# Kernel tuning notes

Hardware: AMD Instinct MI355X
Metric: run time of the kernel (lower is better)

## Reference

```python
import math
import jax, jax.numpy as jnp
import numpy as np

MODEL_DIM = 2048
NUM_HEADS = 16
HEAD_DIM = MODEL_DIM // NUM_HEADS
B, T = 4, 2048


def setup_inputs() -> dict:
    key = jax.random.key(0)
    ks = jax.random.split(key, 9)
    s = 0.02
    d = MODEL_DIM
    return {
        "x": jax.random.normal(ks[0], (B, T, d), dtype=jnp.float32),
        "wq": jax.random.normal(ks[1], (d, d), dtype=jnp.float32) * s,
        "bq": jnp.zeros((d,), dtype=jnp.float32),
        "wk": jax.random.normal(ks[2], (d, d), dtype=jnp.float32) * s,
        "bk": jnp.zeros((d,), dtype=jnp.float32),
        "wv": jax.random.normal(ks[3], (d, d), dtype=jnp.float32) * s,
        "bv": jnp.zeros((d,), dtype=jnp.float32),
        "wo": jax.random.normal(ks[4], (d, d), dtype=jnp.float32) * s,
        "bo": jnp.zeros((d,), dtype=jnp.float32),
    }


def reference(x, wq, bq, wk, bk, wv, bv, wo, bo):
    b, t, d = x.shape
    h, hd = NUM_HEADS, HEAD_DIM
    scale = 1.0 / math.sqrt(hd)
    # torch Linear: y = x @ W^T + b
    q = (x @ wq.T + bq).reshape(b, t, h, hd).transpose(0, 2, 1, 3)  # [B,H,T,hd]
    k = (x @ wk.T + bk).reshape(b, t, h, hd).transpose(0, 2, 1, 3)
    v = (x @ wv.T + bv).reshape(b, t, h, hd).transpose(0, 2, 1, 3)
    scores = jnp.einsum("bhqd,bhkd->bhqk", q, k) * scale  # [B,H,T,T]
    mask = jnp.tril(jnp.ones((t, t), dtype=bool))
    scores = jnp.where(mask[None, None], scores, -jnp.inf)
    probs = jax.nn.softmax(scores, axis=-1)
    out = jnp.einsum("bhqk,bhkd->bhqd", probs, v)  # [B,H,T,hd]
    out = out.transpose(0, 2, 1, 3).reshape(b, t, d)
    out = out @ wo.T + bo
    return (out, k, v)
```

## Files before the change

kernel.cpp:

```cpp
#include <hip/hip_runtime.h>
#include <hip/hip_bf16.h>
#include <stdint.h>

typedef __attribute__((ext_vector_type(8))) short short8;
typedef __attribute__((ext_vector_type(4))) float f32x4;

#define DEVI __device__ __forceinline__

DEVI unsigned short f2bf(float f) {
  union { float f; unsigned int u; } c; c.f = f;
  unsigned int u = c.u;
  u += 0x7fffu + ((u >> 16) & 1u);
  return (unsigned short)(u >> 16);
}

DEVI void gl_lds16(const void* gsrc, void* lds) {
  __builtin_amdgcn_global_load_lds(
      (const __attribute__((address_space(1))) unsigned int*)gsrc,
      (__attribute__((address_space(3))) unsigned int*)lds, 16, 0, 0);
}

#define MFMA(a, b, c) __builtin_amdgcn_mfma_f32_16x16x32_bf16((a), (b), (c), 0, 0, 0)
#define BAR()  __builtin_amdgcn_s_barrier()
#define SCHED0() __builtin_amdgcn_sched_barrier(0)

__global__ void cvt_f32_bf16(const float* __restrict__ in,
                             unsigned short* __restrict__ out, int n4) {
  const int stride = gridDim.x * blockDim.x;
  for (int i = blockIdx.x * blockDim.x + threadIdx.x; i < n4; i += stride) {
    const float4 v = ((const float4*)in)[i];
    ushort4 o;
    o.x = f2bf(v.x); o.y = f2bf(v.y); o.z = f2bf(v.z); o.w = f2bf(v.w);
    ((ushort4*)out)[i] = o;
  }
}

__global__ void cvt_w4(const float* __restrict__ w0, const float* __restrict__ w1,
                       const float* __restrict__ w2, const float* __restrict__ w3,
                       unsigned short* __restrict__ o0, unsigned short* __restrict__ o1,
                       unsigned short* __restrict__ o2, unsigned short* __restrict__ o3,
                       int n4) {
  const int sel = blockIdx.y;
  const float* in = sel == 0 ? w0 : sel == 1 ? w1 : sel == 2 ? w2 : w3;
  unsigned short* out = sel == 0 ? o0 : sel == 1 ? o1 : sel == 2 ? o2 : o3;
  const int stride = gridDim.x * blockDim.x;
  for (int i = blockIdx.x * blockDim.x + threadIdx.x; i < n4; i += stride) {
    const float4 v = ((const float4*)in)[i];
    ushort4 o;
    o.x = f2bf(v.x); o.y = f2bf(v.y); o.z = f2bf(v.z); o.w = f2bf(v.w);
    ((ushort4*)out)[i] = o;
  }
}


template<int MODE>
__global__ __launch_bounds__(512, 2)
void gemm8p(const unsigned short* __restrict__ A,
            const unsigned short* __restrict__ Bw,
            const float* __restrict__ bq,
            const float* __restrict__ bk,
            const float* __restrict__ bv,
            float* __restrict__ Kf,
            float* __restrict__ Vf,
            unsigned short* __restrict__ Qpk,
            unsigned short* __restrict__ Kpk,
            unsigned short* __restrict__ Vpk,
            float* __restrict__ Cf,
            int M, int N, int K)
{
  __shared__ unsigned short S[2][32768];
  const int tid  = threadIdx.x;
  const int lane = tid & 63;
  const int wid  = tid >> 6;
  const int l15  = lane & 15, l4 = lane >> 4;
  const int wm   = wid >> 2, wn = wid & 3;

  const int chunk = gridDim.x >> 3;
  const int q  = blockIdx.x;
  const int wg = (q & 7) * chunk + (q >> 3);
  const int bm = (wg & 31) * 256;
  const int bn = (wg >> 5) * 256;

  const unsigned short* Asrc = A  + (size_t)(bm + (wid >> 1) * 16 + l15) * K + (wid & 1) * 32 + l4 * 8;
  const unsigned short* Bsrc = Bw + (size_t)(bn + (wid >> 1) * 16 + l15) * K + (wid & 1) * 32 + l4 * 8;

  const int nKt   = K >> 6;
  const int HTmax = nKt * 4;

  auto stage_ht = [&](int g) {
    if (g >= HTmax) return;
    const int t = g >> 2, sub = g & 3, buf = t & 1, k0 = t << 6;
#pragma unroll
    for (int cc = 0; cc < 2; ++cc) {
      if (sub >= 2) {
        const int c = (sub - 2) * 2 + cc;
        gl_lds16(Asrc + (size_t)(c * 64) * K + k0,
                 &S[buf][c * 4096 + wid * 512 + lane * 8]);
      } else {
        const int c = sub * 2 + cc;
        gl_lds16(Bsrc + (size_t)(c * 64) * K + k0,
                 &S[buf][16384 + c * 4096 + wid * 512 + lane * 8]);
      }
    }
  };

#pragma unroll
  for (int g = 0; g < 7; ++g) stage_ht(g);
  asm volatile("s_waitcnt vmcnt(6)" ::: "memory");
  SCHED0();
  BAR();

  f32x4 acc[8][4] = {};
  short8 a[4][2], b[4][2];

  for (int t = 0; t < nKt; ++t) {
    const unsigned short* Sb = S[t & 1];
    const int P = t * 4;

#pragma unroll
    for (int i = 0; i < 4; ++i)
#pragma unroll
      for (int ks = 0; ks < 2; ++ks)
        a[i][ks] = *(const short8*)&Sb[((wm * 8 + i) * 2 + ks) * 512 + lane * 8];
#pragma unroll
    for (int j = 0; j < 4; ++j)
#pragma unroll
      for (int ks = 0; ks < 2; ++ks)
        b[j][ks] = *(const short8*)&Sb[16384 + ((wn * 4 + j) * 2 + ks) * 512 + lane * 8];
    stage_ht(P + 7);
    BAR();
    asm volatile("s_waitcnt lgkmcnt(0)" ::: "memory");
    SCHED0();
    __builtin_amdgcn_s_setprio(1);
#pragma unroll
    for (int i = 0; i < 4; ++i)
#pragma unroll
      for (int j = 0; j < 2; ++j)
#pragma unroll
        for (int ks = 0; ks < 2; ++ks)
          acc[i][j] = MFMA(a[i][ks], b[j][ks], acc[i][j]);
    __builtin_amdgcn_s_setprio(0);
    BAR();

    stage_ht(P + 8);
    BAR();
    __builtin_amdgcn_s_setprio(1);
#pragma unroll
    for (int i = 0; i < 4; ++i)
#pragma unroll
      for (int j = 0; j < 2; ++j)
#pragma unroll
        for (int ks = 0; ks < 2; ++ks)
          acc[i][2 + j] = MFMA(a[i][ks], b[2 + j][ks], acc[i][2 + j]);
    __builtin_amdgcn_s_setprio(0);
    BAR();

#pragma unroll
    for (int i = 0; i < 4; ++i)
#pragma unroll
      for (int ks = 0; ks < 2; ++ks)
        a[i][ks] = *(const short8*)&Sb[((wm * 8 + 4 + i) * 2 + ks) * 512 + lane * 8];
    stage_ht(P + 9);
    BAR();
    asm volatile("s_waitcnt lgkmcnt(0)" ::: "memory");
    SCHED0();
    __builtin_amdgcn_s_setprio(1);
#pragma unroll
    for (int i = 0; i < 4; ++i)
#pragma unroll
      for (int j = 0; j < 2; ++j)
#pragma unroll
        for (int ks = 0; ks < 2; ++ks)
          acc[4 + i][j] = MFMA(a[i][ks], b[j][ks], acc[4 + i][j]);
    __builtin_amdgcn_s_setprio(0);
    BAR();

    stage_ht(P + 10);
    if (t < nKt - 2)       { asm volatile("s_waitcnt vmcnt(6)" ::: "memory"); SCHED0(); }
    else if (t == nKt - 2) { asm volatile("s_waitcnt vmcnt(0)" ::: "memory"); SCHED0(); }
    BAR();
    __builtin_amdgcn_s_setprio(1);
#pragma unroll
    for (int i = 0; i < 4; ++i)
#pragma unroll
      for (int j = 0; j < 2; ++j)
#pragma unroll
        for (int ks = 0; ks < 2; ++ks)
          acc[4 + i][2 + j] = MFMA(a[i][ks], b[2 + j][ks], acc[4 + i][2 + j]);
    __builtin_amdgcn_s_setprio(0);
    BAR();
  }

  const int rbase = l4 * 4;
#pragma unroll
  for (int m = 0; m < 8; ++m) {
    const int row0 = bm + wm * 128 + m * 16 + rbase;
#pragma unroll
    for (int n = 0; n < 4; ++n) {
      const int col6 = bn + wn * 64 + n * 16 + l15;
      if constexpr (MODE == 3) {
        const float bb = bq[col6];
#pragma unroll
        for (int r = 0; r < 4; ++r)
          Cf[(size_t)(row0 + r) * N + col6] = acc[m][n][r] + bb;
      } else {
        const int sel = col6 >> 11;
        const int col = col6 & 2047;
        const float bb = (sel == 0 ? bq : sel == 1 ? bk : bv)[col];
        float vv[4];
#pragma unroll
        for (int r = 0; r < 4; ++r) vv[r] = acc[m][n][r] + bb;
        const int bI = row0 >> 11, t0 = row0 & 2047;
        const int h = col >> 7, e = col & 127;
        const size_t hb = ((size_t)(bI * 16 + h)) * 262144;
        if (sel == 0) {
          const size_t qb = hb + (size_t)(t0 >> 4) * 2048 + (e >> 5) * 512
                          + (t0 & 15) * 32 + (e & 31);
#pragma unroll
          for (int r = 0; r < 4; ++r) Qpk[qb + (size_t)r * 32] = f2bf(vv[r]);
        } else if (sel == 1) {
          const size_t idx = hb + (size_t)t0 * 128 + e;
          const size_t qb = hb + (size_t)(t0 >> 4) * 2048 + (e >> 5) * 512
                          + (t0 & 15) * 32 + (e & 31);
#pragma unroll
          for (int r = 0; r < 4; ++r) {
            Kf[idx + (size_t)r * 128] = vv[r];
            Kpk[qb + (size_t)r * 32] = f2bf(vv[r]);
          }
        } else {
          const size_t idx = hb + (size_t)t0 * 128 + e;
#pragma unroll
          for (int r = 0; r < 4; ++r) Vf[idx + (size_t)r * 128] = vv[r];
          const size_t vb = hb + (size_t)(t0 >> 6) * 8192 + (size_t)(e >> 4) * 1024
                          + ((t0 >> 5) & 1) * 512 + (e & 15) * 32 + (t0 & 31);
          ushort4 pk;
          pk.x = f2bf(vv[0]); pk.y = f2bf(vv[1]);
          pk.z = f2bf(vv[2]); pk.w = f2bf(vv[3]);
          *(ushort4*)&Vpk[vb] = pk;
        }
      }
    }
  }
}

__global__ __launch_bounds__(256, 2)
void attn_fwd(const unsigned short* __restrict__ Qf,
              const unsigned short* __restrict__ Kf,
              const unsigned short* __restrict__ Vf,
              unsigned short* __restrict__ Ab)
{
  constexpr float scale = 0.08838834764831843f;
  __shared__ unsigned short Pl[4][32][72];

  const int bid = blockIdx.x;
  const int xcd = bid & 7;
  const int idx = bid >> 3;
  const int bh  = xcd * 8 + (idx & 7);
  const int prI = idx >> 3;
  const int tid = threadIdx.x;
  const int wid = tid >> 6, lane = tid & 63;
  const int p   = prI * 4 + wid;
  const int bI = bh >> 4, h = bh & 15;
  const int lr = lane & 15, lg = lane >> 4;
  const int lfo = lr * 32 + lg * 8;

  const unsigned short* Qh = Qf + (size_t)bh * 262144;
  const unsigned short* Kp = Kf + (size_t)bh * 262144;
  const unsigned short* Vp = Vf + (size_t)bh * 262144;

  for (int pass = 0; pass < 2; ++pass) {
    const int strip = pass ? p : (63 - p);
    const int qw = strip * 32;
    const unsigned short* Qp = Qh + (size_t)(qw >> 4) * 2048;

    short8 qf[2][4];
#pragma unroll
    for (int m = 0; m < 2; ++m)
#pragma unroll
      for (int ks = 0; ks < 4; ++ks)
        qf[m][ks] = *(const short8*)&Qp[m * 2048 + ks * 512 + lfo];

    f32x4 o[2][8] = {};
    float mrun[2][4], lrun[2][4];
#pragma unroll
    for (int m = 0; m < 2; ++m)
#pragma unroll
      for (int r = 0; r < 4; ++r) { mrun[m][r] = -1e30f; lrun[m][r] = 0.f; }

    const int nfull = qw >> 6;
    for (int kt = 0; kt <= nfull; ++kt) {
      const int kv0 = kt * 64;
      const bool diag = (kt == nfull);
      const unsigned short* Kt = Kp + (size_t)(kv0 >> 4) * 2048;
      const unsigned short* Vt = Vp + (size_t)(kv0 >> 6) * 8192;

      short8 kf[4][4];
#pragma unroll
      for (int n = 0; n < 4; ++n)
#pragma unroll
        for (int ks = 0; ks < 4; ++ks)
          kf[n][ks] = *(const short8*)&Kt[n * 2048 + ks * 512 + lfo];
      f32x4 s[2][4] = {};
      __builtin_amdgcn_s_setprio(1);
#pragma unroll
      for (int ks = 0; ks < 4; ++ks)
#pragma unroll
        for (int m = 0; m < 2; ++m)
#pragma unroll
          for (int n = 0; n < 4; ++n)
            s[m][n] = MFMA(qf[m][ks], kf[n][ks], s[m][n]);
      __builtin_amdgcn_s_setprio(0);

      short8 vf[2][8];
#pragma unroll
      for (int ks2 = 0; ks2 < 2; ++ks2)
#pragma unroll
        for (int dt = 0; dt < 8; ++dt)
          vf[ks2][dt] = *(const short8*)&Vt[dt * 1024 + ks2 * 512 + lfo];

      float tmax[2][4];
#pragma unroll
      for (int m = 0; m < 2; ++m)
#pragma unroll
        for (int r = 0; r < 4; ++r) tmax[m][r] = -1e30f;
#pragma unroll
      for (int m = 0; m < 2; ++m)
#pragma unroll
        for (int n = 0; n < 4; ++n) {
          const int kg = kv0 + n * 16 + lr;
#pragma unroll
          for (int r = 0; r < 4; ++r) {
            float sv = s[m][n][r] * scale;
            if (diag) {
              const int qg = qw + m * 16 + lg * 4 + r;
              sv = (kg <= qg) ? sv : -1e30f;
            }
            s[m][n][r] = sv;
            tmax[m][r] = fmaxf(tmax[m][r], sv);
          }
        }
#pragma unroll
      for (int m = 0; m < 2; ++m)
#pragma unroll
        for (int r = 0; r < 4; ++r) {
#pragma unroll
          for (int off = 8; off >= 1; off >>= 1)
            tmax[m][r] = fmaxf(tmax[m][r], __shfl_xor(tmax[m][r], off));
          const float mnew  = fmaxf(mrun[m][r], tmax[m][r]);
          const float alpha = __expf(mrun[m][r] - mnew);
          mrun[m][r] = mnew;
          lrun[m][r] *= alpha;
#pragma unroll
          for (int d = 0; d < 8; ++d) o[m][d][r] *= alpha;
        }
#pragma unroll
      for (int m = 0; m < 2; ++m) {
        float ls[4] = {0.f, 0.f, 0.f, 0.f};
#pragma unroll
        for (int n = 0; n < 4; ++n)
#pragma unroll
          for (int r = 0; r < 4; ++r) {
            const float pv = __expf(s[m][n][r] - mrun[m][r]);
            s[m][n][r] = pv;
            ls[r] += pv;
          }
#pragma unroll
        for (int r = 0; r < 4; ++r) {
#pragma unroll
          for (int off = 8; off >= 1; off >>= 1) ls[r] += __shfl_xor(ls[r], off);
          lrun[m][r] += ls[r];
        }
#pragma unroll
        for (int n = 0; n < 4; ++n)
#pragma unroll
          for (int r = 0; r < 4; ++r)
            Pl[wid][m * 16 + lg * 4 + r][n * 16 + lr] = f2bf(s[m][n][r]);
      }
#pragma unroll
      for (int ks2 = 0; ks2 < 2; ++ks2) {
        short8 pa[2];
#pragma unroll
        for (int m = 0; m < 2; ++m)
          pa[m] = *(const short8*)&Pl[wid][m * 16 + lr][ks2 * 32 + lg * 8];
        __builtin_amdgcn_s_setprio(1);
#pragma unroll
        for (int dt = 0; dt < 8; ++dt)
#pragma unroll
          for (int m = 0; m < 2; ++m)
            o[m][dt] = MFMA(pa[m], vf[ks2][dt], o[m][dt]);
        __builtin_amdgcn_s_setprio(0);
      }
    }
#pragma unroll
    for (int m = 0; m < 2; ++m)
#pragma unroll
      for (int r = 0; r < 4; ++r) {
        const float inv = 1.0f / lrun[m][r];
        const int t = qw + m * 16 + lg * 4 + r;
        unsigned short* dst = Ab + ((size_t)(bI * 2048 + t)) * 2048 + h * 128;
#pragma unroll
        for (int dt = 0; dt < 8; ++dt)
          dst[dt * 16 + lr] = f2bf(o[m][dt][r] * inv);
      }
  }
}

extern "C" void kernel_launch(void* const* d_in, const int* in_sizes, int n_in,
                              void* d_out, int out_size, void* d_ws, size_t ws_size,
                              hipStream_t stream) {
  const float* x  = (const float*)d_in[0];
  const float* wq = (const float*)d_in[1];
  const float* bq = (const float*)d_in[2];
  const float* wk = (const float*)d_in[3];
  const float* bk = (const float*)d_in[4];
  const float* wv = (const float*)d_in[5];
  const float* bv = (const float*)d_in[6];
  const float* wo = (const float*)d_in[7];
  const float* bo = (const float*)d_in[8];

  float* out  = (float*)d_out;
  float* kout = out + (size_t)16777216;
  float* vout = out + (size_t)33554432;

  unsigned short* xb  = (unsigned short*)d_ws;
  unsigned short* wqb = xb  + 16777216;
  unsigned short* wkb = wqb + 4194304;
  unsigned short* wvb = wkb + 4194304;
  unsigned short* wob = wvb + 4194304;
  unsigned short* Qw  = wob + 4194304;
  unsigned short* Kw  = Qw  + 16777216;
  unsigned short* Vfw = Kw  + 16777216;
  unsigned short* Aw  = Vfw + 16777216;

  const int M = 8192, K = 2048;

  cvt_f32_bf16<<<1024, 256, 0, stream>>>(x, xb, 4194304);
  cvt_w4<<<dim3(256, 4), 256, 0, stream>>>(wq, wk, wv, wo,
                                           wqb, wkb, wvb, wob, 1048576);

  gemm8p<0><<<dim3(768), 512, 0, stream>>>(xb, wqb, bq, bk, bv,
                                           kout, vout, Qw, Kw, Vfw,
                                           nullptr, M, 6144, K);

  attn_fwd<<<dim3(512), 256, 0, stream>>>(Qw, Kw, Vfw, Aw);

  gemm8p<3><<<dim3(256), 512, 0, stream>>>(Aw, wob, bo, nullptr, nullptr,
                                           nullptr, nullptr, nullptr, nullptr, nullptr,
                                           out, M, 2048, K);
}
```

Before: 522.6 us.

## Replace 256x256 LDS GEMM with 128x128 tiles reading pre-packed weights directly

Weights are converted to bf16 and packed into an MFMA-fragment-friendly blocked layout. The GEMM then shrinks to 128x128 tiles with 256 threads, stages only A through LDS, and loads B fragments straight from global memory. This drops the B LDS traffic and the deep multi-stage pipeline, and launches four times as many workgroups. In exchange it loses the 256x256 register reuse and the pipelining, issues many more global loads for B, and waits on vmcnt(0) every iteration.

```diff
diff --git a/kernel.cpp b/kernel.cpp
--- a/kernel.cpp
+++ b/kernel.cpp
@@ -35,166 +35,109 @@
   }
 }
 
-__global__ void cvt_w4(const float* __restrict__ w0, const float* __restrict__ w1,
-                       const float* __restrict__ w2, const float* __restrict__ w3,
-                       unsigned short* __restrict__ o0, unsigned short* __restrict__ o1,
-                       unsigned short* __restrict__ o2, unsigned short* __restrict__ o3,
-                       int n4) {
+__global__ void cvt_wpack4(const float* __restrict__ w0, const float* __restrict__ w1,
+                           const float* __restrict__ w2, const float* __restrict__ w3,
+                           unsigned short* __restrict__ o0, unsigned short* __restrict__ o1,
+                           unsigned short* __restrict__ o2, unsigned short* __restrict__ o3,
+                           int n4) {
   const int sel = blockIdx.y;
   const float* in = sel == 0 ? w0 : sel == 1 ? w1 : sel == 2 ? w2 : w3;
   unsigned short* out = sel == 0 ? o0 : sel == 1 ? o1 : sel == 2 ? o2 : o3;
   const int stride = gridDim.x * blockDim.x;
   for (int i = blockIdx.x * blockDim.x + threadIdx.x; i < n4; i += stride) {
+    const int n = i >> 9;
+    const int k = (i & 511) * 4;
     const float4 v = ((const float4*)in)[i];
     ushort4 o;
     o.x = f2bf(v.x); o.y = f2bf(v.y); o.z = f2bf(v.z); o.w = f2bf(v.w);
-    ((ushort4*)out)[i] = o;
+    const size_t dst = (size_t)(n >> 4) * 32768 + (k >> 5) * 512
+                     + (n & 15) * 32 + (k & 31);
+    *(ushort4*)&out[dst] = o;
   }
 }
 
 
 template<int MODE>
-__global__ __launch_bounds__(512, 2)
-void gemm8p(const unsigned short* __restrict__ A,
-            const unsigned short* __restrict__ Bw,
-            const float* __restrict__ bq,
-            const float* __restrict__ bk,
-            const float* __restrict__ bv,
-            float* __restrict__ Kf,
-            float* __restrict__ Vf,
-            unsigned short* __restrict__ Qpk,
-            unsigned short* __restrict__ Kpk,
-            unsigned short* __restrict__ Vpk,
-            float* __restrict__ Cf,
-            int M, int N, int K)
+__global__ __launch_bounds__(256, 2)
+void gemm_bd(const unsigned short* __restrict__ A,
+             const unsigned short* __restrict__ Bpk,
+             const float* __restrict__ bq,
+             const float* __restrict__ bk,
+             const float* __restrict__ bv,
+             float* __restrict__ Kf,
+             float* __restrict__ Vf,
+             unsigned short* __restrict__ Qpk,
+             unsigned short* __restrict__ Kpk,
+             unsigned short* __restrict__ Vpk,
+             float* __restrict__ Cf,
+             int M, int N, int K)
 {
-  __shared__ unsigned short S[2][32768];
+  __shared__ unsigned short S[2][8192];
   const int tid  = threadIdx.x;
   const int lane = tid & 63;
   const int wid  = tid >> 6;
   const int l15  = lane & 15, l4 = lane >> 4;
-  const int wm   = wid >> 2, wn = wid & 3;
+  const int wm   = wid >> 1, wn = wid & 1;
+  const int lfo  = l15 * 32 + l4 * 8;
 
   const int chunk = gridDim.x >> 3;
   const int q  = blockIdx.x;
   const int wg = (q & 7) * chunk + (q >> 3);
-  const int bm = (wg & 31) * 256;
-  const int bn = (wg >> 5) * 256;
-
-  const unsigned short* Asrc = A  + (size_t)(bm + (wid >> 1) * 16 + l15) * K + (wid & 1) * 32 + l4 * 8;
-  const unsigned short* Bsrc = Bw + (size_t)(bn + (wid >> 1) * 16 + l15) * K + (wid & 1) * 32 + l4 * 8;
-
-  const int nKt   = K >> 6;
-  const int HTmax = nKt * 4;
-
-  auto stage_ht = [&](int g) {
-    if (g >= HTmax) return;
-    const int t = g >> 2, sub = g & 3, buf = t & 1, k0 = t << 6;
-#pragma unroll
-    for (int cc = 0; cc < 2; ++cc) {
-      if (sub >= 2) {
-        const int c = (sub - 2) * 2 + cc;
-        gl_lds16(Asrc + (size_t)(c * 64) * K + k0,
-                 &S[buf][c * 4096 + wid * 512 + lane * 8]);
-      } else {
-        const int c = sub * 2 + cc;
-        gl_lds16(Bsrc + (size_t)(c * 64) * K + k0,
-                 &S[buf][16384 + c * 4096 + wid * 512 + lane * 8]);
-      }
-    }
-  };
-
-#pragma unroll
-  for (int g = 0; g < 7; ++g) stage_ht(g);
-  asm volatile("s_waitcnt vmcnt(6)" ::: "memory");
+  const int mb = M >> 7;
+  const int bm = (wg % mb) * 128;
+  const int bn = (wg / mb) * 128;
+  const int bn4 = bn >> 4;
+
+  const int nT = K >> 6;
+
+#define STAGEA(t_, buf_) do {                                               \
+    _Pragma("unroll")                                                       \
+    for (int r = 0; r < 4; ++r) {                                           \
+      const int f = r * 4 + wid;                                            \
+      gl_lds16(A + (size_t)(bm + (f >> 1) * 16 + l15) * K                   \
+                 + (t_) * 64 + (f & 1) * 32 + l4 * 8,                       \
+               &S[buf_][f * 512 + lane * 8]);                               \
+    }                                                                       \
+  } while (0)
+
+  STAGEA(0, 0);
+  asm volatile("s_waitcnt vmcnt(0)" ::: "memory");
   SCHED0();
   BAR();
 
-  f32x4 acc[8][4] = {};
-  short8 a[4][2], b[4][2];
-
-  for (int t = 0; t < nKt; ++t) {
+  f32x4 acc[4][4] = {};
+
+  for (int t = 0; t < nT; ++t) {
+    if (t + 1 < nT) STAGEA(t + 1, (t + 1) & 1);
     const unsigned short* Sb = S[t & 1];
-    const int P = t * 4;
-
-#pragma unroll
-    for (int i = 0; i < 4; ++i)
-#pragma unroll
-      for (int ks = 0; ks < 2; ++ks)
-        a[i][ks] = *(const short8*)&Sb[((wm * 8 + i) * 2 + ks) * 512 + lane * 8];
-#pragma unroll
-    for (int j = 0; j < 4; ++j)
-#pragma unroll
-      for (int ks = 0; ks < 2; ++ks)
-        b[j][ks] = *(const short8*)&Sb[16384 + ((wn * 4 + j) * 2 + ks) * 512 + lane * 8];
-    stage_ht(P + 7);
+#pragma unroll
+    for (int ks = 0; ks < 2; ++ks) {
+      short8 bfr[4], afr[4];
+#pragma unroll
+      for (int j = 0; j < 4; ++j)
+        bfr[j] = *(const short8*)&Bpk[(size_t)(bn4 + wn * 4 + j) * 32768
+                                      + (t * 2 + ks) * 512 + lfo];
+#pragma unroll
+      for (int i = 0; i < 4; ++i)
+        afr[i] = *(const short8*)&Sb[((wm * 4 + i) * 2 + ks) * 512 + lane * 8];
+      __builtin_amdgcn_s_setprio(1);
+#pragma unroll
+      for (int i = 0; i < 4; ++i)
+#pragma unroll
+        for (int j = 0; j < 4; ++j)
+          acc[i][j] = MFMA(afr[i], bfr[j], acc[i][j]);
+      __builtin_amdgcn_s_setprio(0);
+    }
+    asm volatile("s_waitcnt vmcnt(0)" ::: "memory");
+    SCHED0();
     BAR();
-    asm volatile("s_waitcnt lgkmcnt(0)" ::: "memory");
-    SCHED0();
-    __builtin_amdgcn_s_setprio(1);
-#pragma unroll
-    for (int i = 0; i < 4; ++i)
-#pragma unroll
-      for (int j = 0; j < 2; ++j)
-#pragma unroll
-        for (int ks = 0; ks < 2; ++ks)
-          acc[i][j] = MFMA(a[i][ks], b[j][ks], acc[i][j]);
-    __builtin_amdgcn_s_setprio(0);
-    BAR();
-
-    stage_ht(P + 8);
-    BAR();
-    __builtin_amdgcn_s_setprio(1);
-#pragma unroll
-    for (int i = 0; i < 4; ++i)
-#pragma unroll
-      for (int j = 0; j < 2; ++j)
-#pragma unroll
-        for (int ks = 0; ks < 2; ++ks)
-          acc[i][2 + j] = MFMA(a[i][ks], b[2 + j][ks], acc[i][2 + j]);
-    __builtin_amdgcn_s_setprio(0);
-    BAR();
-
-#pragma unroll
-    for (int i = 0; i < 4; ++i)
-#pragma unroll
-      for (int ks = 0; ks < 2; ++ks)
-        a[i][ks] = *(const short8*)&Sb[((wm * 8 + 4 + i) * 2 + ks) * 512 + lane * 8];
-    stage_ht(P + 9);
-    BAR();
-    asm volatile("s_waitcnt lgkmcnt(0)" ::: "memory");
-    SCHED0();
-    __builtin_amdgcn_s_setprio(1);
-#pragma unroll
-    for (int i = 0; i < 4; ++i)
-#pragma unroll
-      for (int j = 0; j < 2; ++j)
-#pragma unroll
-        for (int ks = 0; ks < 2; ++ks)
-          acc[4 + i][j] = MFMA(a[i][ks], b[j][ks], acc[4 + i][j]);
-    __builtin_amdgcn_s_setprio(0);
-    BAR();
-
-    stage_ht(P + 10);
-    if (t < nKt - 2)       { asm volatile("s_waitcnt vmcnt(6)" ::: "memory"); SCHED0(); }
-    else if (t == nKt - 2) { asm volatile("s_waitcnt vmcnt(0)" ::: "memory"); SCHED0(); }
-    BAR();
-    __builtin_amdgcn_s_setprio(1);
-#pragma unroll
-    for (int i = 0; i < 4; ++i)
-#pragma unroll
-      for (int j = 0; j < 2; ++j)
-#pragma unroll
-        for (int ks = 0; ks < 2; ++ks)
-          acc[4 + i][2 + j] = MFMA(a[i][ks], b[2 + j][ks], acc[4 + i][2 + j]);
-    __builtin_amdgcn_s_setprio(0);
-    BAR();
-  }
+  }
+#undef STAGEA
 
   const int rbase = l4 * 4;
 #pragma unroll
-  for (int m = 0; m < 8; ++m) {
-    const int row0 = bm + wm * 128 + m * 16 + rbase;
+  for (int m = 0; m < 4; ++m) {
+    const int row0 = bm + wm * 64 + m * 16 + rbase;
 #pragma unroll
     for (int n = 0; n < 4; ++n) {
       const int col6 = bn + wn * 64 + n * 16 + l15;
@@ -435,16 +378,16 @@
   const int M = 8192, K = 2048;
 
   cvt_f32_bf16<<<1024, 256, 0, stream>>>(x, xb, 4194304);
-  cvt_w4<<<dim3(256, 4), 256, 0, stream>>>(wq, wk, wv, wo,
-                                           wqb, wkb, wvb, wob, 1048576);
-
-  gemm8p<0><<<dim3(768), 512, 0, stream>>>(xb, wqb, bq, bk, bv,
-                                           kout, vout, Qw, Kw, Vfw,
-                                           nullptr, M, 6144, K);
+  cvt_wpack4<<<dim3(256, 4), 256, 0, stream>>>(wq, wk, wv, wo,
+                                               wqb, wkb, wvb, wob, 1048576);
+
+  gemm_bd<0><<<dim3(3072), 256, 0, stream>>>(xb, wqb, bq, bk, bv,
+                                             kout, vout, Qw, Kw, Vfw,
+                                             nullptr, M, 6144, K);
 
   attn_fwd<<<dim3(512), 256, 0, stream>>>(Qw, Kw, Vfw, Aw);
 
-  gemm8p<3><<<dim3(256), 512, 0, stream>>>(Aw, wob, bo, nullptr, nullptr,
-                                           nullptr, nullptr, nullptr, nullptr, nullptr,
-                                           out, M, 2048, K);
-}
+  gemm_bd<3><<<dim3(1024), 256, 0, stream>>>(Aw, wob, bo, nullptr, nullptr,
+                                             nullptr, nullptr, nullptr, nullptr, nullptr,
+                                             out, M, 2048, K);
+}
```

Result: slower. 724.9 us (+38.7%).
